# Kernel optimization log

Measured on AMD Instinct MI355X. Metric: run time of the kernel, lower is better.

## Reference

```python
import jax, jax.numpy as jnp
import numpy as np

IN_DIM, OUT_DIM, N_PROTO, RANK = 1024, 1024, 32, 16


def setup_inputs() -> dict:
    key = jax.random.key(0)
    ks = jax.random.split(key, 5)
    x = jax.random.normal(ks[0], (2, 4096, IN_DIM), dtype=jnp.float32)
    prototypes = jax.random.normal(ks[1], (N_PROTO, IN_DIM), dtype=jnp.float32) * 0.02
    B = jax.random.normal(ks[2], (N_PROTO, RANK, IN_DIM), dtype=jnp.float32) * 0.02
    A = jax.random.normal(ks[3], (N_PROTO, OUT_DIM, RANK), dtype=jnp.float32) * 0.02
    bias = jnp.zeros((N_PROTO, OUT_DIM), dtype=jnp.float32)
    temp = jnp.asarray(1.0, dtype=jnp.float32)
    return {"x": x, "prototypes": prototypes, "B": B, "A": A, "bias": bias, "temp": temp}


def reference(x, prototypes, B, A, bias, temp):
    lead = x.shape[:-1]
    xf = x.reshape(-1, IN_DIM)                       # [N, in]
    x2 = jnp.sum(xf * xf, axis=1, keepdims=True)     # [N,1]
    p2 = jnp.sum(prototypes * prototypes, axis=1)    # [P]
    d2 = x2 + p2[None, :] - 2.0 * (xf @ prototypes.T)
    dists = jnp.sqrt(jnp.maximum(d2, 0.0))           # [N,P]
    t = jnp.maximum(jnp.abs(temp), 0.1)
    w = jax.nn.softmax(-dists / t, axis=1)           # [N,P]
    topw, topi = jax.lax.top_k(w, 2)                 # [N,2]
    topw = topw / jnp.sum(topw, axis=1, keepdims=True)
    out = jnp.zeros((xf.shape[0], OUT_DIM), dtype=xf.dtype)
    for tslot in range(2):
        idx = topi[:, tslot]                          # [N]
        wt = topw[:, tslot:tslot + 1]                 # [N,1]
        h = jnp.einsum('nri,ni->nr', B[idx], xf)      # gathered low-rank down-proj
        y = jnp.einsum('nor,nr->no', A[idx], h) + bias[idx]
        out = out + wt * y
    return out.reshape(*lead, OUT_DIM)
```

## Files before the change

### kernel.cpp

```cpp
#include <hip/hip_runtime.h>
#include <math.h>

#define ROWS_TOTAL 8192
#define KDIM 1024
#define NPROTO 32
#define RNK 16
#define OUTD 1024
#define TIE_EPS 1.30e-4
#define DELTA 4.0e-5f
#define FLAG_CAP 4096

__device__ __forceinline__ unsigned short f2bf(float v) {
    unsigned int b = __float_as_uint(v);
    return (unsigned short)((b + 0x7FFFu + ((b >> 16) & 1u)) >> 16);
}

__global__ __launch_bounds__(256) void prep_kernel(
    const float* __restrict__ A, const float* __restrict__ B,
    const float* __restrict__ proto, float* __restrict__ At,
    float* __restrict__ Bt, unsigned short* __restrict__ Bt16,
    float* __restrict__ Pt, double* __restrict__ p2g,
    int* __restrict__ counts, int* __restrict__ flagcnt)
{
    __shared__ float T[16 * 68];
    __shared__ float U[64 * 20];
    __shared__ double red[32][9];
    __shared__ float TP[32][33];
    const int tid = threadIdx.x;

    if (blockIdx.x < 128) {
        const int p = blockIdx.x >> 2;
        const int c0 = (blockIdx.x & 3) * 4;
        const float4* B4 = (const float4*)(B + (size_t)p * RNK * KDIM);
        const float4* A4 = (const float4*)(A + (size_t)p * OUTD * RNK);
        float4* Bt4 = (float4*)(Bt + (size_t)p * KDIM * RNK);
        float4* At4 = (float4*)(At + (size_t)p * RNK * OUTD);
        unsigned short* Bt16p = Bt16 + (size_t)p * KDIM * RNK;
        for (int c = c0; c < c0 + 4; ++c) {
            {
                int r = tid >> 4, kk = tid & 15;
                float4 v = B4[r * 256 + c * 16 + kk];
                *(float4*)&T[r * 68 + kk * 4] = v;
            }
            {
                int o = tid >> 2, rq = tid & 3;
                float4 v = A4[(c * 64 + o) * 4 + rq];
                *(float4*)&U[o * 20 + rq * 4] = v;
            }
            __syncthreads();
            {
                int k = tid >> 2, rq = tid & 3;
                float4 g = make_float4(T[(rq * 4 + 0) * 68 + k], T[(rq * 4 + 1) * 68 + k],
                                       T[(rq * 4 + 2) * 68 + k], T[(rq * 4 + 3) * 68 + k]);
                Bt4[(c * 64 + k) * 4 + rq] = g;
                unsigned int lo = (unsigned int)f2bf(g.x) | ((unsigned int)f2bf(g.y) << 16);
                unsigned int hi = (unsigned int)f2bf(g.z) | ((unsigned int)f2bf(g.w) << 16);
                *(uint2*)(Bt16p + (size_t)(c * 64 + k) * 16 + rq * 4) = make_uint2(lo, hi);
            }
            {
                int r = tid >> 4, ow = tid & 15;
                float4 g = make_float4(U[(ow * 4 + 0) * 20 + r], U[(ow * 4 + 1) * 20 + r],
                                       U[(ow * 4 + 2) * 20 + r], U[(ow * 4 + 3) * 20 + r]);
                At4[r * 256 + c * 16 + ow] = g;
            }
            __syncthreads();
        }
    } else {
        const int qb = blockIdx.x - 128;
        if (qb == 0) {
            if (tid < 64) counts[tid] = 0;
            if (tid == 64) flagcnt[0] = 0;
            {
                const int p = tid >> 3, seg = tid & 7;
                const float* a = proto + (size_t)p * KDIM + seg * 128;
                double s = 0.0;
                for (int k = 0; k < 128; ++k) {
                    double v = (double)a[k];
                    s = fma(v, v, s);
                }
                red[p][seg] = s;
            }
            __syncthreads();
            if (tid < 32) {
                double acc = red[tid][0];
                #pragma unroll
                for (int j = 1; j < 8; ++j) acc += red[tid][j];
                p2g[tid] = acc;
            }
        }
        float4* Pt4 = (float4*)Pt;
        for (int kc = qb * 8; kc < qb * 8 + 8; ++kc) {
            {
                int cc = tid >> 3, kk4 = tid & 7;
                float4 v = *(const float4*)(proto + (size_t)cc * KDIM + kc * 32 + kk4 * 4);
                TP[cc][kk4 * 4 + 0] = v.x; TP[cc][kk4 * 4 + 1] = v.y;
                TP[cc][kk4 * 4 + 2] = v.z; TP[cc][kk4 * 4 + 3] = v.w;
            }
            __syncthreads();
            {
                int kk = tid >> 3, c4 = tid & 7;
                float4 g = make_float4(TP[c4 * 4 + 0][kk], TP[c4 * 4 + 1][kk],
                                       TP[c4 * 4 + 2][kk], TP[c4 * 4 + 3][kk]);
                Pt4[(kc * 32 + kk) * 8 + c4] = g;
            }
            __syncthreads();
        }
    }
}

#define INS(kb, ib) { \
    bool lt1 = (kb) < k1, lt2 = (kb) < k2, lt3 = (kb) < k3, lt4 = (kb) < k4; \
    float nk4 = lt3 ? k3 : (lt4 ? (kb) : k4); int ni4 = lt3 ? i3 : (lt4 ? (ib) : i4); \
    float nk3 = lt2 ? k2 : (lt3 ? (kb) : k3); int ni3 = lt2 ? i2 : (lt3 ? (ib) : i3); \
    float nk2 = lt1 ? k1 : (lt2 ? (kb) : k2); int ni2 = lt1 ? i1 : (lt2 ? (ib) : i2); \
    k4 = nk4; i4 = ni4; k3 = nk3; i3 = ni3; k2 = nk2; i2 = ni2; \
    if (lt1) { k1 = (kb); i1 = (ib); } }

__global__ __launch_bounds__(256) void route_kernel(
    const float* __restrict__ x, const float* __restrict__ Pt,
    const float* __restrict__ temp, const double* __restrict__ p2g,
    float4* __restrict__ route, int* __restrict__ counts,
    int* __restrict__ flagcnt, int* __restrict__ flaglist)
{
    __shared__ float Xs[8 * KDIM];
    __shared__ float part[4][8][33];
    __shared__ float x2p[4][8];
    __shared__ int lcnt[64];

    const int tid = threadIdx.x;
    const int w = tid >> 6, l = tid & 63;
    const int c4 = l & 7, kslot = l >> 3;
    const int rowbase = blockIdx.x * 8;

    if (tid < 64) lcnt[tid] = 0;

    const float4* x4 = (const float4*)x;
    float sq[8];
    #pragma unroll
    for (int j = 0; j < 8; ++j) {
        float4 v = x4[(size_t)rowbase * 256 + j * 256 + tid];
        ((float4*)Xs)[j * 256 + tid] = v;
        sq[j] = fmaf(v.x, v.x, fmaf(v.y, v.y, fmaf(v.z, v.z, v.w * v.w)));
    }
    #pragma unroll
    for (int m = 1; m < 64; m <<= 1) {
        #pragma unroll
        for (int j = 0; j < 8; ++j) sq[j] += __shfl_xor(sq[j], m);
    }
    if (l == 0) {
        #pragma unroll
        for (int j = 0; j < 8; ++j) x2p[w][j] = sq[j];
    }
    __syncthreads();

    float acc[8][4];
    #pragma unroll
    for (int j = 0; j < 8; ++j)
        #pragma unroll
        for (int jj = 0; jj < 4; ++jj) acc[j][jj] = 0.f;

    const float4* Pt4 = (const float4*)Pt;
    const int kbase = w * 256;
    #pragma unroll 4
    for (int i = 0; i < 32; ++i) {
        const int k = kbase + i * 8 + kslot;
        float4 pv = Pt4[k * 8 + c4];
        #pragma unroll
        for (int j = 0; j < 8; ++j) {
            float xv = Xs[j * KDIM + k];
            acc[j][0] = fmaf(xv, pv.x, acc[j][0]);
            acc[j][1] = fmaf(xv, pv.y, acc[j][1]);
            acc[j][2] = fmaf(xv, pv.z, acc[j][2]);
            acc[j][3] = fmaf(xv, pv.w, acc[j][3]);
        }
    }
    #pragma unroll
    for (int m = 8; m < 64; m <<= 1) {
        #pragma unroll
        for (int j = 0; j < 8; ++j) {
            acc[j][0] += __shfl_xor(acc[j][0], m);
            acc[j][1] += __shfl_xor(acc[j][1], m);
            acc[j][2] += __shfl_xor(acc[j][2], m);
            acc[j][3] += __shfl_xor(acc[j][3], m);
        }
    }
    if (kslot == 0) {
        #pragma unroll
        for (int j = 0; j < 8; ++j) {
            part[w][j][4 * c4 + 0] = acc[j][0];
            part[w][j][4 * c4 + 1] = acc[j][1];
            part[w][j][4 * c4 + 2] = acc[j][2];
            part[w][j][4 * c4 + 3] = acc[j][3];
        }
    }
    __syncthreads();

    {
        const int rowsel = tid >> 5, c = tid & 31;
        float dsum = (part[0][rowsel][c] + part[1][rowsel][c])
                   + (part[2][rowsel][c] + part[3][rowsel][c]);
        float key = (float)(p2g[c] - 2.0 * (double)dsum);
        float x2 = (x2p[0][rowsel] + x2p[1][rowsel])
                 + (x2p[2][rowsel] + x2p[3][rowsel]);

        float k1 = key, k2 = 3.0e38f, k3 = 3.1e38f, k4 = 3.2e38f;
        int i1 = c, i2 = 64, i3 = 65, i4 = 66;
        #pragma unroll
        for (int m = 1; m < 32; m <<= 1) {
            float b1 = __shfl_xor(k1, m), b2 = __shfl_xor(k2, m);
            float b3 = __shfl_xor(k3, m), b4 = __shfl_xor(k4, m);
            int j1 = __shfl_xor(i1, m), j2 = __shfl_xor(i2, m);
            int j3 = __shfl_xor(i3, m), j4 = __shfl_xor(i4, m);
            INS(b1, j1); INS(b2, j2); INS(b3, j3); INS(b4, j4);
        }
        if (c == 0) {
            const int row = rowbase + rowsel;
            const float tf = fmaxf(fabsf(temp[0]), 0.1f);
            bool amb = (k2 - k1 < DELTA) || (k3 - k2 < DELTA)
                    || (fabsf((k3 - k2) - (float)TIE_EPS) < DELTA)
                    || (k4 - k3 < DELTA);
            bool tie = (k3 - k2) < (float)TIE_EPS;
            bool take3 = tie && (i3 < i2);
            float ksel = take3 ? k3 : k2;
            int   isel = take3 ? i3 : i2;
            float d0 = sqrtf(fmaxf(x2 + k1, 0.f));
            float d1 = sqrtf(fmaxf(x2 + ksel, 0.f));
            float e = expf((d0 - d1) / tf);
            float w0 = 1.f / (1.f + e);
            route[row] = make_float4(__int_as_float(i1), __int_as_float(isel),
                                     w0, e * w0);
            atomicAdd(&lcnt[i1], 1);
            atomicAdd(&lcnt[32 + isel], 1);
            if (amb) {
                int fi = atomicAdd(flagcnt, 1);
                if (fi < FLAG_CAP) flaglist[fi] = row;
            }
        }
    }
    __syncthreads();
    if (tid < 64) atomicAdd(&counts[tid], lcnt[tid]);
}

__global__ __launch_bounds__(256) void refine_scan_kernel(
    const float* __restrict__ x, const float* __restrict__ proto,
    const float* __restrict__ temp, const double* __restrict__ p2g,
    float4* __restrict__ route, int* __restrict__ counts,
    const int* __restrict__ flagcnt, const int* __restrict__ flaglist,
    int2* __restrict__ segs)
{
    const int tid = threadIdx.x;
    const int w = tid >> 6, l = tid & 63;
    const int c = l & 31, half = l >> 5;
    const int n = min(flagcnt[0], FLAG_CAP);

    for (int f = w; f < n; f += 4) {
        const int row = flaglist[f];
        const float* xr = x + (size_t)row * KDIM;
        double xs = 0.0;
        for (int k = l * 16; k < l * 16 + 16; ++k) {
            double v = (double)xr[k];
            xs = fma(v, v, xs);
        }
        #pragma unroll
        for (int m = 1; m < 64; m <<= 1) xs += __shfl_xor(xs, m);
        const float* pr = proto + (size_t)c * KDIM + half * 512;
        const float* xh = xr + half * 512;
        double d0a = 0.0, d1a = 0.0;
        for (int k = 0; k < 512; k += 2) {
            d0a = fma((double)xh[k], (double)pr[k], d0a);
            d1a = fma((double)xh[k + 1], (double)pr[k + 1], d1a);
        }
        double acc = d0a + d1a;
        acc += __shfl_xor(acc, 32);
        double key = p2g[c] - 2.0 * acc;

        double k1 = key, k2 = 1.0e300, k3 = 1.1e300;
        int i1 = c, i2 = 64, i3 = 65;
        #pragma unroll
        for (int m = 1; m < 32; m <<= 1) {
            double b1 = __shfl_xor(k1, m), b2 = __shfl_xor(k2, m), b3 = __shfl_xor(k3, m);
            int j1 = __shfl_xor(i1, m), j2 = __shfl_xor(i2, m), j3 = __shfl_xor(i3, m);
            bool c1 = (k1 < b1) || (k1 == b1 && i1 < j1);
            double m1 = c1 ? k1 : b1, M1 = c1 ? b1 : k1;
            int mi1 = c1 ? i1 : j1, Mi1 = c1 ? j1 : i1;
            bool c2 = (k2 < b2) || (k2 == b2 && i2 < j2);
            double m2 = c2 ? k2 : b2;
            int mi2 = c2 ? i2 : j2;
            bool c3 = (k3 < b3) || (k3 == b3 && i3 < j3);
            double m3 = c3 ? k3 : b3;
            int mi3 = c3 ? i3 : j3;
            bool c4 = (M1 < m2) || (M1 == m2 && Mi1 < mi2);
            double t2 = c4 ? M1 : m2, T2 = c4 ? m2 : M1;
            int ti2 = c4 ? Mi1 : mi2, Ti2 = c4 ? mi2 : Mi1;
            bool c5 = (T2 < m3) || (T2 == m3 && Ti2 < mi3);
            k1 = m1; i1 = mi1;
            k2 = t2; i2 = ti2;
            k3 = c5 ? T2 : m3; i3 = c5 ? Ti2 : mi3;
        }
        if (l == 0) {
            const double tmp = (double)fmaxf(fabsf(temp[0]), 0.1f);
            bool tie = (k3 - k2) < TIE_EPS;
            bool take3 = tie && (i3 < i2);
            double ksel = take3 ? k3 : k2;
            int isel = take3 ? i3 : i2;
            double dd0 = sqrt(fmax(xs + k1, 0.0));
            double dd1 = sqrt(fmax(xs + ksel, 0.0));
            float e = expf((float)((dd0 - dd1) / tmp));
            float w0 = 1.f / (1.f + e);
            float4 old = route[row];
            int oi1 = __float_as_int(old.x), oisel = __float_as_int(old.y);
            if (oi1 != i1) { atomicAdd(&counts[oi1], -1); atomicAdd(&counts[i1], 1); }
            if (oisel != isel) { atomicAdd(&counts[32 + oisel], -1); atomicAdd(&counts[32 + isel], 1); }
            route[row] = make_float4(__int_as_float(i1), __int_as_float(isel),
                                     w0, e * w0);
        }
    }
    __syncthreads();
    if (tid < 64) {
        int v = atomicAdd(&counts[tid], 0);
        int sum = v;
        #pragma unroll
        for (int off = 1; off < 32; off <<= 1) {
            int u = __shfl_up(sum, off, 32);
            if ((tid & 31) >= off) sum += u;
        }
        counts[tid] = sum - v;
        segs[tid] = make_int2(sum - v, sum);
    }
}

__global__ __launch_bounds__(256) void scatter_kernel(
    const float4* __restrict__ route, int* __restrict__ counts,
    int* __restrict__ rowlist0, int* __restrict__ rowlist1)
{
    __shared__ int lcnt[64];
    __shared__ int gbase[64];
    const int tid = threadIdx.x;
    const int i = blockIdx.x * 256 + tid;
    if (tid < 64) lcnt[tid] = 0;
    __syncthreads();
    float4 rt = route[i];
    int p0 = __float_as_int(rt.x);
    int p1 = __float_as_int(rt.y);
    int lp0 = atomicAdd(&lcnt[p0], 1);
    int lp1 = atomicAdd(&lcnt[32 + p1], 1);
    __syncthreads();
    if (tid < 64) gbase[tid] = atomicAdd(&counts[tid], lcnt[tid]);
    __syncthreads();
    rowlist0[gbase[p0] + lp0] = i;
    rowlist1[gbase[32 + p1] + lp1] = i;
}

__global__ __launch_bounds__(256) void h_kernel(
    const float* __restrict__ x, const unsigned short* __restrict__ Bt16,
    const float4* __restrict__ route, float* __restrict__ hws)
{
    __shared__ float Xs[8 * KDIM];
    __shared__ int ps[16];

    const int tid = threadIdx.x;
    const int rowbase = blockIdx.x * 8;

    const float4* x4 = (const float4*)x;
    #pragma unroll
    for (int j = 0; j < 8; ++j)
        ((float4*)Xs)[j * 256 + tid] = x4[(size_t)rowbase * 256 + j * 256 + tid];
    if (tid < 16) {
        float4 rt = route[rowbase + (tid >> 1)];
        ps[tid] = __float_as_int((tid & 1) ? rt.y : rt.x);
    }
    __syncthreads();

    const int pair = tid >> 4;
    const int kslot = (tid >> 2) & 3;
    const int r4 = tid & 3;
    const int rrow = pair >> 1, slot = pair & 1;
    const unsigned short* Bp = Bt16 + (size_t)ps[pair] * KDIM * RNK + r4 * 4;
    const float* Xr = &Xs[rrow * KDIM];

    float4 acc = {0.f, 0.f, 0.f, 0.f};
    #pragma unroll 8
    for (int i = 0; i < 256; ++i) {
        const int k = i * 4 + kslot;
        float xv = Xr[k];
        uint2 bv = *(const uint2*)(Bp + (size_t)k * 16);
        float b0 = __uint_as_float((bv.x & 0xFFFFu) << 16);
        float b1 = __uint_as_float(bv.x & 0xFFFF0000u);
        float b2 = __uint_as_float((bv.y & 0xFFFFu) << 16);
        float b3 = __uint_as_float(bv.y & 0xFFFF0000u);
        acc.x = fmaf(xv, b0, acc.x);
        acc.y = fmaf(xv, b1, acc.y);
        acc.z = fmaf(xv, b2, acc.z);
        acc.w = fmaf(xv, b3, acc.w);
    }
    #pragma unroll
    for (int msk = 4; msk < 16; msk <<= 1) {
        acc.x += __shfl_xor(acc.x, msk);
        acc.y += __shfl_xor(acc.y, msk);
        acc.z += __shfl_xor(acc.z, msk);
        acc.w += __shfl_xor(acc.w, msk);
    }
    if (kslot == 0)
        *(float4*)(hws + (size_t)(slot * ROWS_TOTAL + rowbase + rrow) * 16 + r4 * 4) = acc;
}

__global__ __launch_bounds__(256) void y_kernel(
    const float* __restrict__ At, const float* __restrict__ bias,
    const float4* __restrict__ route, const int* __restrict__ rowlist,
    const int2* __restrict__ segs, const float* __restrict__ hws,
    float* __restrict__ out, int slot)
{
    __shared__ float hsm[16][17];
    __shared__ int rows[16];
    __shared__ float wts[16];

    const int tid = threadIdx.x;
    const int f4 = tid;
    const int p = blockIdx.y;
    const int2 sg = segs[slot * 32 + p];
    const float4* Atp = (const float4*)(At + (size_t)p * RNK * OUTD);
    const float4 bb = ((const float4*)(bias + (size_t)p * OUTD))[f4];

    float4 Areg[16];
    #pragma unroll
    for (int r = 0; r < 16; ++r) Areg[r] = Atp[r * 256 + f4];

    for (int c = blockIdx.x; ; c += gridDim.x) {
        const int base = sg.x + c * 16;
        if (base >= sg.y) break;
        const int m = min(16, sg.y - base);

        if (tid < 16) {
            int rr = rowlist[base + min(tid, m - 1)];
            rows[tid] = rr;
            float4 rt = route[rr];
            wts[tid] = slot ? rt.w : rt.z;
        }
        __syncthreads();
        {
            const int e = tid >> 4, r = tid & 15;
            hsm[e][r] = hws[(size_t)(slot * ROWS_TOTAL + rows[e]) * 16 + r];
        }
        __syncthreads();

        for (int e = 0; e < m; ++e) {
            float4 acc = bb;
            #pragma unroll
            for (int r = 0; r < 16; ++r) {
                float hr = hsm[e][r];
                acc.x = fmaf(hr, Areg[r].x, acc.x);
                acc.y = fmaf(hr, Areg[r].y, acc.y);
                acc.z = fmaf(hr, Areg[r].z, acc.z);
                acc.w = fmaf(hr, Areg[r].w, acc.w);
            }
            const float w = wts[e];
            float4 v = make_float4(w * acc.x, w * acc.y, w * acc.z, w * acc.w);
            float4* dst = (float4*)(out + (size_t)rows[e] * OUTD) + f4;
            if (slot) {
                float4 old = *dst;
                v.x += old.x; v.y += old.y; v.z += old.z; v.w += old.w;
            }
            *dst = v;
        }
        __syncthreads();
    }
}

extern "C" void kernel_launch(void* const* d_in, const int* in_sizes, int n_in,
                              void* d_out, int out_size, void* d_ws, size_t ws_size,
                              hipStream_t stream) {
    const float* x     = (const float*)d_in[0];
    const float* proto = (const float*)d_in[1];
    const float* B     = (const float*)d_in[2];
    const float* A     = (const float*)d_in[3];
    const float* bias  = (const float*)d_in[4];
    const float* temp  = (const float*)d_in[5];
    float* out = (float*)d_out;

    char* wsb = (char*)d_ws;
    float4* route = (float4*)wsb;
    int* rowlist0 = (int*)(wsb + 131072);
    int* rowlist1 = rowlist0 + ROWS_TOTAL;
    int* counts   = (int*)(wsb + 196608);
    int2* segs    = (int2*)(wsb + 196864);
    double* p2g   = (double*)(wsb + 197376);
    int* flagcnt  = (int*)(wsb + 197632);
    int* flaglist = (int*)(wsb + 197760);
    float* Pt     = (float*)(wsb + 262144);
    float* Bt     = (float*)(wsb + 393216);
    float* At     = (float*)(wsb + 393216 + 2097152);
    float* hws    = (float*)(wsb + 393216 + 2 * 2097152);
    unsigned short* Bt16 = (unsigned short*)(wsb + 393216 + 3 * 2097152);

    prep_kernel<<<132, 256, 0, stream>>>(A, B, proto, At, Bt, Bt16, Pt, p2g,
                                         counts, flagcnt);
    route_kernel<<<ROWS_TOTAL / 8, 256, 0, stream>>>(x, Pt, temp, p2g, route,
                                                     counts, flagcnt, flaglist);
    refine_scan_kernel<<<1, 256, 0, stream>>>(x, proto, temp, p2g, route,
                                              counts, flagcnt, flaglist, segs);
    scatter_kernel<<<ROWS_TOTAL / 256, 256, 0, stream>>>(route, counts, rowlist0, rowlist1);
    h_kernel<<<ROWS_TOTAL / 8, 256, 0, stream>>>(x, Bt16, route, hws);
    y_kernel<<<dim3(16, NPROTO), 256, 0, stream>>>(At, bias, route, rowlist0, segs, hws, out, 0);
    y_kernel<<<dim3(16, NPROTO), 256, 0, stream>>>(At, bias, route, rowlist1, segs, hws, out, 1);
}
```

Measured before the change: 150.7 us.

## Fuse low-rank down-projection into routing kernel and drop separate h kernel

Moves the gathered B-projection (h computation) into route_kernel, reusing the x rows already held in shared memory. This removes the h_kernel launch and its second full read of x (32 MB). Because the refine pass can change a row's selected prototypes, refine_scan_kernel now recomputes h for flagged rows whose index changed. The recompute runs serially in a single block, which adds cost when many rows are flagged, and the larger route_kernel may lose some occupancy.

```diff
diff --git a/kernel.cpp b/kernel.cpp
--- a/kernel.cpp
+++ b/kernel.cpp
@@ -119,17 +119,20 @@
 __global__ __launch_bounds__(256) void route_kernel(
     const float* __restrict__ x, const float* __restrict__ Pt,
     const float* __restrict__ temp, const double* __restrict__ p2g,
-    float4* __restrict__ route, int* __restrict__ counts,
-    int* __restrict__ flagcnt, int* __restrict__ flaglist)
+    const unsigned short* __restrict__ Bt16,
+    float4* __restrict__ route, float* __restrict__ hws,
+    int* __restrict__ counts, int* __restrict__ flagcnt,
+    int* __restrict__ flaglist)
 {
     __shared__ float Xs[8 * KDIM];
     __shared__ float part[4][8][33];
     __shared__ float x2p[4][8];
     __shared__ int lcnt[64];
+    __shared__ int ps[16];
 
     const int tid = threadIdx.x;
     const int w = tid >> 6, l = tid & 63;
-    const int c4 = l & 7, kslot = l >> 3;
+    const int c4 = l & 7, kslot8 = l >> 3;
     const int rowbase = blockIdx.x * 8;
 
     if (tid < 64) lcnt[tid] = 0;
@@ -153,44 +156,46 @@
     }
     __syncthreads();
 
-    float acc[8][4];
-    #pragma unroll
-    for (int j = 0; j < 8; ++j)
-        #pragma unroll
-        for (int jj = 0; jj < 4; ++jj) acc[j][jj] = 0.f;
-
-    const float4* Pt4 = (const float4*)Pt;
-    const int kbase = w * 256;
-    #pragma unroll 4
-    for (int i = 0; i < 32; ++i) {
-        const int k = kbase + i * 8 + kslot;
-        float4 pv = Pt4[k * 8 + c4];
-        #pragma unroll
-        for (int j = 0; j < 8; ++j) {
-            float xv = Xs[j * KDIM + k];
-            acc[j][0] = fmaf(xv, pv.x, acc[j][0]);
-            acc[j][1] = fmaf(xv, pv.y, acc[j][1]);
-            acc[j][2] = fmaf(xv, pv.z, acc[j][2]);
-            acc[j][3] = fmaf(xv, pv.w, acc[j][3]);
-        }
-    }
-    #pragma unroll
-    for (int m = 8; m < 64; m <<= 1) {
-        #pragma unroll
-        for (int j = 0; j < 8; ++j) {
-            acc[j][0] += __shfl_xor(acc[j][0], m);
-            acc[j][1] += __shfl_xor(acc[j][1], m);
-            acc[j][2] += __shfl_xor(acc[j][2], m);
-            acc[j][3] += __shfl_xor(acc[j][3], m);
-        }
-    }
-    if (kslot == 0) {
-        #pragma unroll
-        for (int j = 0; j < 8; ++j) {
-            part[w][j][4 * c4 + 0] = acc[j][0];
-            part[w][j][4 * c4 + 1] = acc[j][1];
-            part[w][j][4 * c4 + 2] = acc[j][2];
-            part[w][j][4 * c4 + 3] = acc[j][3];
+    {
+        float acc[8][4];
+        #pragma unroll
+        for (int j = 0; j < 8; ++j)
+            #pragma unroll
+            for (int jj = 0; jj < 4; ++jj) acc[j][jj] = 0.f;
+
+        const float4* Pt4 = (const float4*)Pt;
+        const int kbase = w * 256;
+        #pragma unroll 4
+        for (int i = 0; i < 32; ++i) {
+            const int k = kbase + i * 8 + kslot8;
+            float4 pv = Pt4[k * 8 + c4];
+            #pragma unroll
+            for (int j = 0; j < 8; ++j) {
+                float xv = Xs[j * KDIM + k];
+                acc[j][0] = fmaf(xv, pv.x, acc[j][0]);
+                acc[j][1] = fmaf(xv, pv.y, acc[j][1]);
+                acc[j][2] = fmaf(xv, pv.z, acc[j][2]);
+                acc[j][3] = fmaf(xv, pv.w, acc[j][3]);
+            }
+        }
+        #pragma unroll
+        for (int m = 8; m < 64; m <<= 1) {
+            #pragma unroll
+            for (int j = 0; j < 8; ++j) {
+                acc[j][0] += __shfl_xor(acc[j][0], m);
+                acc[j][1] += __shfl_xor(acc[j][1], m);
+                acc[j][2] += __shfl_xor(acc[j][2], m);
+                acc[j][3] += __shfl_xor(acc[j][3], m);
+            }
+        }
+        if (kslot8 == 0) {
+            #pragma unroll
+            for (int j = 0; j < 8; ++j) {
+                part[w][j][4 * c4 + 0] = acc[j][0];
+                part[w][j][4 * c4 + 1] = acc[j][1];
+                part[w][j][4 * c4 + 2] = acc[j][2];
+                part[w][j][4 * c4 + 3] = acc[j][3];
+            }
         }
     }
     __syncthreads();
@@ -229,6 +234,8 @@
             float w0 = 1.f / (1.f + e);
             route[row] = make_float4(__int_as_float(i1), __int_as_float(isel),
                                      w0, e * w0);
+            ps[2 * rowsel + 0] = i1;
+            ps[2 * rowsel + 1] = isel;
             atomicAdd(&lcnt[i1], 1);
             atomicAdd(&lcnt[32 + isel], 1);
             if (amb) {
@@ -239,14 +246,49 @@
     }
     __syncthreads();
     if (tid < 64) atomicAdd(&counts[tid], lcnt[tid]);
+
+    {
+        const int pair = tid >> 4;
+        const int kslot = (tid >> 2) & 3;
+        const int r4 = tid & 3;
+        const int rrow = pair >> 1, slot = pair & 1;
+        const unsigned short* Bp = Bt16 + (size_t)ps[pair] * KDIM * RNK + r4 * 4;
+        const float* Xr = &Xs[rrow * KDIM];
+
+        float4 acc = {0.f, 0.f, 0.f, 0.f};
+        #pragma unroll 8
+        for (int i = 0; i < 256; ++i) {
+            const int k = i * 4 + kslot;
+            float xv = Xr[k];
+            uint2 bv = *(const uint2*)(Bp + (size_t)k * 16);
+            float b0 = __uint_as_float((bv.x & 0xFFFFu) << 16);
+            float b1 = __uint_as_float(bv.x & 0xFFFF0000u);
+            float b2 = __uint_as_float((bv.y & 0xFFFFu) << 16);
+            float b3 = __uint_as_float(bv.y & 0xFFFF0000u);
+            acc.x = fmaf(xv, b0, acc.x);
+            acc.y = fmaf(xv, b1, acc.y);
+            acc.z = fmaf(xv, b2, acc.z);
+            acc.w = fmaf(xv, b3, acc.w);
+        }
+        #pragma unroll
+        for (int msk = 4; msk < 16; msk <<= 1) {
+            acc.x += __shfl_xor(acc.x, msk);
+            acc.y += __shfl_xor(acc.y, msk);
+            acc.z += __shfl_xor(acc.z, msk);
+            acc.w += __shfl_xor(acc.w, msk);
+        }
+        if (kslot == 0)
+            *(float4*)(hws + (size_t)(slot * ROWS_TOTAL + rowbase + rrow) * 16 + r4 * 4) = acc;
+    }
 }
 
 __global__ __launch_bounds__(256) void refine_scan_kernel(
     const float* __restrict__ x, const float* __restrict__ proto,
     const float* __restrict__ temp, const double* __restrict__ p2g,
-    float4* __restrict__ route, int* __restrict__ counts,
-    const int* __restrict__ flagcnt, const int* __restrict__ flaglist,
-    int2* __restrict__ segs)
+    const unsigned short* __restrict__ Bt16,
+    float4* __restrict__ route, float* __restrict__ hws,
+    int* __restrict__ counts, const int* __restrict__ flagcnt,
+    const int* __restrict__ flaglist, int2* __restrict__ segs)
 {
     const int tid = threadIdx.x;
     const int w = tid >> 6, l = tid & 63;
@@ -297,22 +339,42 @@
             k2 = t2; i2 = ti2;
             k3 = c5 ? T2 : m3; i3 = c5 ? Ti2 : mi3;
         }
+        bool tie = (k3 - k2) < TIE_EPS;
+        bool take3 = tie && (i3 < i2);
+        int isel = take3 ? i3 : i2;
+        double ksel = take3 ? k3 : k2;
+
+        float4 old = route[row];
+        int oi1 = __float_as_int(old.x), oisel = __float_as_int(old.y);
+
         if (l == 0) {
             const double tmp = (double)fmaxf(fabsf(temp[0]), 0.1f);
-            bool tie = (k3 - k2) < TIE_EPS;
-            bool take3 = tie && (i3 < i2);
-            double ksel = take3 ? k3 : k2;
-            int isel = take3 ? i3 : i2;
             double dd0 = sqrt(fmax(xs + k1, 0.0));
             double dd1 = sqrt(fmax(xs + ksel, 0.0));
             float e = expf((float)((dd0 - dd1) / tmp));
             float w0 = 1.f / (1.f + e);
-            float4 old = route[row];
-            int oi1 = __float_as_int(old.x), oisel = __float_as_int(old.y);
             if (oi1 != i1) { atomicAdd(&counts[oi1], -1); atomicAdd(&counts[i1], 1); }
             if (oisel != isel) { atomicAdd(&counts[32 + oisel], -1); atomicAdd(&counts[32 + isel], 1); }
             route[row] = make_float4(__int_as_float(i1), __int_as_float(isel),
                                      w0, e * w0);
+        }
+        #pragma unroll
+        for (int sl = 0; sl < 2; ++sl) {
+            int np = sl ? isel : i1;
+            int op = sl ? oisel : oi1;
+            if (np != op) {
+                const int r = l & 15, kq = l >> 4;
+                const unsigned short* Bp = Bt16 + (size_t)np * KDIM * RNK + r;
+                float hacc = 0.f;
+                for (int k = kq * 256; k < kq * 256 + 256; ++k) {
+                    unsigned int bu = (unsigned int)Bp[(size_t)k * 16] << 16;
+                    hacc = fmaf(xr[k], __uint_as_float(bu), hacc);
+                }
+                hacc += __shfl_xor(hacc, 16);
+                hacc += __shfl_xor(hacc, 32);
+                if (kq == 0)
+                    hws[(size_t)(sl * ROWS_TOTAL + row) * 16 + r] = hacc;
+            }
         }
     }
     __syncthreads();
@@ -349,59 +411,6 @@
     __syncthreads();
     rowlist0[gbase[p0] + lp0] = i;
     rowlist1[gbase[32 + p1] + lp1] = i;
-}
-
-__global__ __launch_bounds__(256) void h_kernel(
-    const float* __restrict__ x, const unsigned short* __restrict__ Bt16,
-    const float4* __restrict__ route, float* __restrict__ hws)
-{
-    __shared__ float Xs[8 * KDIM];
-    __shared__ int ps[16];
-
-    const int tid = threadIdx.x;
-    const int rowbase = blockIdx.x * 8;
-
-    const float4* x4 = (const float4*)x;
-    #pragma unroll
-    for (int j = 0; j < 8; ++j)
-        ((float4*)Xs)[j * 256 + tid] = x4[(size_t)rowbase * 256 + j * 256 + tid];
-    if (tid < 16) {
-        float4 rt = route[rowbase + (tid >> 1)];
-        ps[tid] = __float_as_int((tid & 1) ? rt.y : rt.x);
-    }
-    __syncthreads();
-
-    const int pair = tid >> 4;
-    const int kslot = (tid >> 2) & 3;
-    const int r4 = tid & 3;
-    const int rrow = pair >> 1, slot = pair & 1;
-    const unsigned short* Bp = Bt16 + (size_t)ps[pair] * KDIM * RNK + r4 * 4;
-    const float* Xr = &Xs[rrow * KDIM];
-
-    float4 acc = {0.f, 0.f, 0.f, 0.f};
-    #pragma unroll 8
-    for (int i = 0; i < 256; ++i) {
-        const int k = i * 4 + kslot;
-        float xv = Xr[k];
-        uint2 bv = *(const uint2*)(Bp + (size_t)k * 16);
-        float b0 = __uint_as_float((bv.x & 0xFFFFu) << 16);
-        float b1 = __uint_as_float(bv.x & 0xFFFF0000u);
-        float b2 = __uint_as_float((bv.y & 0xFFFFu) << 16);
-        float b3 = __uint_as_float(bv.y & 0xFFFF0000u);
-        acc.x = fmaf(xv, b0, acc.x);
-        acc.y = fmaf(xv, b1, acc.y);
-        acc.z = fmaf(xv, b2, acc.z);
-        acc.w = fmaf(xv, b3, acc.w);
-    }
-    #pragma unroll
-    for (int msk = 4; msk < 16; msk <<= 1) {
-        acc.x += __shfl_xor(acc.x, msk);
-        acc.y += __shfl_xor(acc.y, msk);
-        acc.z += __shfl_xor(acc.z, msk);
-        acc.w += __shfl_xor(acc.w, msk);
-    }
-    if (kslot == 0)
-        *(float4*)(hws + (size_t)(slot * ROWS_TOTAL + rowbase + rrow) * 16 + r4 * 4) = acc;
 }
 
 __global__ __launch_bounds__(256) void y_kernel(
@@ -494,12 +503,13 @@
 
     prep_kernel<<<132, 256, 0, stream>>>(A, B, proto, At, Bt, Bt16, Pt, p2g,
                                          counts, flagcnt);
-    route_kernel<<<ROWS_TOTAL / 8, 256, 0, stream>>>(x, Pt, temp, p2g, route,
-                                                     counts, flagcnt, flaglist);
-    refine_scan_kernel<<<1, 256, 0, stream>>>(x, proto, temp, p2g, route,
-                                              counts, flagcnt, flaglist, segs);
+    route_kernel<<<ROWS_TOTAL / 8, 256, 0, stream>>>(x, Pt, temp, p2g, Bt16,
+                                                     route, hws, counts,
+                                                     flagcnt, flaglist);
+    refine_scan_kernel<<<1, 256, 0, stream>>>(x, proto, temp, p2g, Bt16,
+                                              route, hws, counts, flagcnt,
+                                              flaglist, segs);
     scatter_kernel<<<ROWS_TOTAL / 256, 256, 0, stream>>>(route, counts, rowlist0, rowlist1);
-    h_kernel<<<ROWS_TOTAL / 8, 256, 0, stream>>>(x, Bt16, route, hws);
     y_kernel<<<dim3(16, NPROTO), 256, 0, stream>>>(At, bias, route, rowlist0, segs, hws, out, 0);
     y_kernel<<<dim3(16, NPROTO), 256, 0, stream>>>(At, bias, route, rowlist1, segs, hws, out, 1);
 }
```

Measured after the change: 143.4 us (median of 2 runs). 4.8% less time.
